# Kernel tuning notes

Measured on AMD Instinct MI355X. Metric: run time of the kernel, lower is better.

The kernel has to match this reference:

```python
import jax, jax.numpy as jnp
import numpy as np

HEADS = 2
C1 = 33    # per-head out channels, conv1
C2 = 550   # per-head out channels, conv2


def _lin_params(key, fan_in, fan_out):
    kw, kb = jax.random.split(key)
    scale = 1.0 / np.sqrt(fan_in)
    W = jax.random.uniform(kw, (fan_in, fan_out), jnp.float32, -scale, scale)
    b = jax.random.uniform(kb, (fan_out,), jnp.float32, -scale, scale)
    return W, b


def transformer_conv(x, src, dst, Wq, bq, Wk, bk, Wv, bv, Ws, bs, heads, out_ch):
    """PyG TransformerConv (concat=True, root_weight=True, beta=False)."""
    N = x.shape[0]
    q = (x @ Wq + bq).reshape(N, heads, out_ch)  # query of target node i
    k = (x @ Wk + bk).reshape(N, heads, out_ch)  # key of source node j
    v = (x @ Wv + bv).reshape(N, heads, out_ch)  # value of source node j
    # attention logits per edge: [E, H]
    alpha = jnp.einsum('ehc,ehc->eh', q[dst], k[src]) / jnp.sqrt(jnp.float32(out_ch))
    # segment softmax over incoming edges of each dst node
    m = jax.lax.stop_gradient(jax.ops.segment_max(alpha, dst, num_segments=N))  # [N,H]
    e = jnp.exp(alpha - m[dst])
    denom = jax.ops.segment_sum(e, dst, num_segments=N)  # [N,H]
    a = e / denom[dst]
    # weighted scatter-aggregate of source values: [N,H,C]
    out = jax.ops.segment_sum(a[..., None] * v[src], dst, num_segments=N)
    out = out.reshape(N, heads * out_ch)
    # root/skip connection
    out = out + x @ Ws + bs
    return out


def setup_inputs() -> dict:
    key = jax.random.key(0)
    ks = jax.random.split(key, 10)
    N, E, IN = 20000, 120000, 256
    x = jax.random.normal(ks[0], (N, IN), jnp.float32)
    edge_index = jax.random.randint(ks[1], (2, E), 0, N, jnp.int64 if jax.config.jax_enable_x64 else jnp.int32)
    d = {'x': x, 'edge_index': edge_index}
    # conv1: IN -> heads*C1
    d['Wq1'], d['bq1'] = _lin_params(ks[2], IN, HEADS * C1)
    d['Wk1'], d['bk1'] = _lin_params(ks[3], IN, HEADS * C1)
    d['Wv1'], d['bv1'] = _lin_params(ks[4], IN, HEADS * C1)
    d['Ws1'], d['bs1'] = _lin_params(ks[5], IN, HEADS * C1)
    # conv2: heads*C1 -> heads*C2
    IN2 = HEADS * C1
    d['Wq2'], d['bq2'] = _lin_params(ks[6], IN2, HEADS * C2)
    d['Wk2'], d['bk2'] = _lin_params(ks[7], IN2, HEADS * C2)
    d['Wv2'], d['bv2'] = _lin_params(ks[8], IN2, HEADS * C2)
    d['Ws2'], d['bs2'] = _lin_params(ks[9], IN2, HEADS * C2)
    return d


def reference(x, edge_index, Wq1, bq1, Wk1, bk1, Wv1, bv1, Ws1, bs1,
              Wq2, bq2, Wk2, bk2, Wv2, bv2, Ws2, bs2):
    src, dst = edge_index[0], edge_index[1]
    h = transformer_conv(x, src, dst, Wq1, bq1, Wk1, bk1, Wv1, bv1, Ws1, bs1, HEADS, C1)
    h = transformer_conv(h, src, dst, Wq2, bq2, Wk2, bk2, Wv2, bv2, Ws2, bs2, HEADS, C2)
    # x.view(N, 550, heads).max(dim=2) -- faithful to the original reshape layout
    h = h.reshape(h.shape[0], C2, HEADS)
    return jnp.max(h, axis=2)
```

## Files before the change

### kernel.cpp

```cpp
#include <hip/hip_runtime.h>
#include <math.h>

#define HEADS 2
#define C1    33
#define C2    550
#define D1    66
#define D2    1100
#define IN1   256
#define PROJW 288
#define KU    224
#define KZ    96
#define ZW    144
#define AUW   232

typedef __attribute__((ext_vector_type(8))) short bfrag;
typedef __attribute__((ext_vector_type(4))) float f32x4;

__device__ inline unsigned short f2bf(float f) {
    unsigned int u = __float_as_uint(f);
    u += 0x7FFFu + ((u >> 16) & 1u);
    return (unsigned short)(u >> 16);
}

__device__ inline int xcd_slot(int bid, int slots) {
    return (bid >> 3) + (bid & 7) * slots;
}

__global__ void k_prep1(const float* __restrict__ Wq, const float* __restrict__ bq,
                        const float* __restrict__ Wk, const float* __restrict__ bk,
                        const float* __restrict__ Wv, const float* __restrict__ bv,
                        const float* __restrict__ Ws, const float* __restrict__ bs,
                        unsigned short* __restrict__ Wt1, float* __restrict__ bcat) {
    int bid = blockIdx.x;
    int lk = bid & 3, t = bid >> 2;
    int ks = t & 7, g = t >> 3;
    int col = threadIdx.x;
    int c = g * 96 + col;
    int k0 = ks * 32 + lk * 8;
    short vals[8];
    float bia = 0.f;
    if (c < 4 * D1) {
        int m = c / D1, j = c % D1;
        const float* W; const float* B;
        switch (m) {
            case 0: W = Wq; B = bq; break;
            case 1: W = Wk; B = bk; break;
            case 2: W = Wv; B = bv; break;
            default: W = Ws; B = bs; break;
        }
        #pragma unroll
        for (int e = 0; e < 8; e++) vals[e] = (short)f2bf(W[(size_t)(k0 + e) * D1 + j]);
        bia = B[j];
    } else {
        #pragma unroll
        for (int e = 0; e < 8; e++) vals[e] = 0;
    }
    *(bfrag*)&Wt1[((size_t)bid * 96 + col) * 8] = *(bfrag*)vals;
    if (ks == 0 && lk == 0) bcat[c] = bia;
}

__global__ void k_prep2(const float* __restrict__ Wv2, const float* __restrict__ bv2,
                        const float* __restrict__ Ws2, const float* __restrict__ bs2,
                        unsigned short* __restrict__ W2t) {
    int bid = blockIdx.x;
    int lk = bid & 3, t = bid >> 2;
    int ks = t % 7, g = t / 7;
    int col = threadIdx.x;
    int c = g * 96 + col;
    int k0 = ks * 32 + lk * 8;
    short vals[8];
    #pragma unroll
    for (int e = 0; e < 8; e++) {
        int k = k0 + e;
        float val = 0.f;
        if (c < D2) {
            if (c < C2) {
                if (k < 66) val = Wv2[(size_t)k * D2 + c];
                else if (k >= 132 && k < 198) val = Ws2[(size_t)(k - 132) * D2 + c];
                else if (k == 198) val = bv2[c];
                else if (k == 223) val = bs2[c];
            } else {
                if (k >= 66 && k < 132) val = Wv2[(size_t)(k - 66) * D2 + c];
                else if (k >= 132 && k < 198) val = Ws2[(size_t)(k - 132) * D2 + c];
                else if (k == 199) val = bv2[c];
                else if (k == 223) val = bs2[c];
            }
        }
        vals[e] = (short)f2bf(val);
    }
    *(bfrag*)&W2t[((size_t)bid * 96 + col) * 8] = *(bfrag*)vals;
}

__global__ void k_hist(const int* __restrict__ dst, int E, int* __restrict__ cnt) {
    int e = blockIdx.x * blockDim.x + threadIdx.x;
    if (e < E) atomicAdd(&cnt[dst[e]], 1);
}

__global__ void k_scan(const int* __restrict__ cnt, int* __restrict__ roff,
                       int* __restrict__ pos, int N) {
    __shared__ int wsum[16];
    __shared__ int carry_s;
    int tid = threadIdx.x, wid = tid >> 6, lane = tid & 63;
    if (tid == 0) { carry_s = 0; roff[0] = 0; }
    __syncthreads();
    for (int base = 0; base < N; base += 1024) {
        int i = base + tid;
        int v = (i < N) ? cnt[i] : 0;
        int x = v;
        #pragma unroll
        for (int s = 1; s < 64; s <<= 1) {
            int t = __shfl_up(x, s, 64);
            if (lane >= s) x += t;
        }
        if (lane == 63) wsum[wid] = x;
        __syncthreads();
        if (tid < 16) {
            int y = wsum[tid];
            #pragma unroll
            for (int s = 1; s < 16; s <<= 1) {
                int t = __shfl_up(y, s, 16);
                if (tid >= s) y += t;
            }
            wsum[tid] = y;
        }
        __syncthreads();
        int carry = carry_s;
        int incl = carry + (wid ? wsum[wid - 1] : 0) + x;
        if (i < N) { roff[i + 1] = incl; pos[i] = incl - v; }
        __syncthreads();
        if (tid == 0) carry_s = carry + wsum[15];
        __syncthreads();
    }
}

__global__ void k_fill(const int* __restrict__ src, const int* __restrict__ dst, int E,
                       int* __restrict__ pos, int* __restrict__ elist) {
    int e = blockIdx.x * blockDim.x + threadIdx.x;
    if (e < E) {
        int slot = atomicAdd(&pos[dst[e]], 1);
        elist[slot] = src[e];
    }
}

__global__ __launch_bounds__(256) void k_precomp(
        const float* __restrict__ Wq2, const float* __restrict__ bq2,
        const float* __restrict__ Wk2, const float* __restrict__ bk2,
        unsigned short* __restrict__ GBt, float* __restrict__ cc) {
    int wave = threadIdx.x >> 6, lane = threadIdx.x & 63;
    int j = blockIdx.x * 4 + wave;
    if (j >= 8978) return;
    const float *u, *v;
    int h = 0, a = 0, b = 0;
    if (j < 8976) {
        h = j / 4488;
        int r = j % 4488;
        a = r / 68; b = r % 68;
        if (b < 66)      { u = Wq2 + (size_t)a * D2 + h * C2; v = Wk2 + (size_t)b * D2 + h * C2; }
        else if (b == 66){ u = Wq2 + (size_t)a * D2 + h * C2; v = bk2 + h * C2; }
        else             { u = Wk2 + (size_t)a * D2 + h * C2; v = bq2 + h * C2; }
    } else {
        h = j - 8976;
        u = bq2 + h * C2; v = bk2 + h * C2;
    }
    float acc = 0.f;
    for (int c = lane; c < C2; c += 64) acc += u[c] * v[c];
    #pragma unroll
    for (int off = 32; off >= 1; off >>= 1) acc += __shfl_xor(acc, off, 64);
    if (lane == 0) {
        if (j < 8976) {
            int r, k;
            if (b < 66)      { r = h * 66 + a; k = b; }
            else if (b == 66){ r = 132 + h;    k = a; }
            else             { r = 134 + h;    k = a; }
            int g = r / 96, cm = r % 96;
            int ks2 = k >> 5, rem = k & 31, lk2 = rem >> 3, e = rem & 7;
            GBt[(((size_t)(g * 3 + ks2) * 4 + lk2) * 96 + cm) * 8 + e] = f2bf(acc);
        } else {
            cc[h] = acc;
        }
    }
}

__global__ __launch_bounds__(256) void k_mm1(
        const float* __restrict__ X, const unsigned short* __restrict__ B,
        const float* __restrict__ bias, float* __restrict__ proj, int N,
        int nRow, int slots) {
    int s = xcd_slot(blockIdx.x, slots);
    if (s >= nRow * 3) return;
    int rowt = s / 3, g = s - rowt * 3;
    int cbase = g * 96;
    int wave = threadIdx.x >> 6, lane = threadIdx.x & 63;
    int lr = lane & 15, lk = lane >> 4;
    int rbase = rowt * 128 + wave * 32;
    int ar[2];
    #pragma unroll
    for (int mi = 0; mi < 2; mi++) {
        int r = rbase + mi * 16 + lr;
        ar[mi] = (r < N) ? r : (N - 1);
    }
    bfrag a[2][8];
    #pragma unroll
    for (int mi = 0; mi < 2; mi++)
        #pragma unroll
        for (int ks = 0; ks < 8; ks++) {
            const float* p = X + (size_t)ar[mi] * IN1 + ks * 32 + lk * 8;
            float4 v0 = *(const float4*)p;
            float4 v1 = *(const float4*)(p + 4);
            bfrag r;
            r[0] = (short)f2bf(v0.x); r[1] = (short)f2bf(v0.y);
            r[2] = (short)f2bf(v0.z); r[3] = (short)f2bf(v0.w);
            r[4] = (short)f2bf(v1.x); r[5] = (short)f2bf(v1.y);
            r[6] = (short)f2bf(v1.z); r[7] = (short)f2bf(v1.w);
            a[mi][ks] = r;
        }
    f32x4 acc[2][6];
    #pragma unroll
    for (int mi = 0; mi < 2; mi++)
        #pragma unroll
        for (int ni = 0; ni < 6; ni++) acc[mi][ni] = (f32x4){0.f, 0.f, 0.f, 0.f};
    #pragma unroll
    for (int ks = 0; ks < 8; ks++) {
        bfrag b[6];
        #pragma unroll
        for (int ni = 0; ni < 6; ni++)
            b[ni] = *(const bfrag*)(B + (size_t)(g * 8 + ks) * 3072 + lk * 768 + (ni * 16 + lr) * 8);
        #pragma unroll
        for (int mi = 0; mi < 2; mi++)
            #pragma unroll
            for (int ni = 0; ni < 6; ni++)
                acc[mi][ni] = __builtin_amdgcn_mfma_f32_16x16x32_bf16(a[mi][ks], b[ni], acc[mi][ni], 0, 0, 0);
    }
    #pragma unroll
    for (int mi = 0; mi < 2; mi++) {
        #pragma unroll
        for (int ni = 0; ni < 6; ni++) {
            int col = cbase + ni * 16 + lr;
            float bia = bias[col];
            #pragma unroll
            for (int r = 0; r < 4; r++) {
                int row = rbase + mi * 16 + lk * 4 + r;
                if (row < N) proj[(size_t)row * PROJW + col] = acc[mi][ni][r] + bia;
            }
        }
    }
}

__global__ __launch_bounds__(128) void k_conv1(
        const float* __restrict__ proj, const int* __restrict__ roff,
        const int* __restrict__ elist, float* __restrict__ h1,
        unsigned short* __restrict__ h1b, int N) {
    int n = blockIdx.x;
    int h = threadIdx.x >> 6;
    int lane = threadIdx.x & 63;
    int half = lane >> 5, l32 = lane & 31;
    size_t pb = (size_t)n * PROJW;
    int hc = h * C1;
    float q_a = proj[pb + hc + l32];
    float q_b = (l32 == 0) ? proj[pb + hc + 32] : 0.f;
    int E0 = roff[n], E1 = roff[n + 1];
    float m = -INFINITY, lsum = 0.f, aca = 0.f, acb = 0.f;
    const float isc = 0.17407765595569785f;
    int i = E0 + half;
    for (; i + 2 < E1; i += 4) {
        int s0 = elist[i], s1 = elist[i + 2];
        size_t b0 = (size_t)s0 * PROJW, b1 = (size_t)s1 * PROJW;
        float k0a = proj[b0 + 66 + hc + l32];
        float k0b = (l32 == 0) ? proj[b0 + 66 + hc + 32] : 0.f;
        float k1a = proj[b1 + 66 + hc + l32];
        float k1b = (l32 == 0) ? proj[b1 + 66 + hc + 32] : 0.f;
        float v0a = proj[b0 + 132 + hc + l32];
        float v0b = (l32 == 0) ? proj[b0 + 132 + hc + 32] : 0.f;
        float v1a = proj[b1 + 132 + hc + l32];
        float v1b = (l32 == 0) ? proj[b1 + 132 + hc + 32] : 0.f;
        float p0 = q_a * k0a + q_b * k0b;
        float p1 = q_a * k1a + q_b * k1b;
        #pragma unroll
        for (int off = 16; off >= 1; off >>= 1) {
            p0 += __shfl_xor(p0, off, 32);
            p1 += __shfl_xor(p1, off, 32);
        }
        float a0 = p0 * isc, a1 = p1 * isc;
        float mp = fmaxf(a0, a1);
        float e0 = __expf(a0 - mp), e1 = __expf(a1 - mp);
        float lp = e0 + e1;
        float apa = e0 * v0a + e1 * v1a;
        float apb = e0 * v0b + e1 * v1b;
        float mnew = fmaxf(m, mp);
        float sc = __expf(m - mnew), sp = __expf(mp - mnew);
        lsum = lsum * sc + lp * sp;
        aca = aca * sc + apa * sp;
        acb = acb * sc + apb * sp;
        m = mnew;
    }
    for (; i < E1; i += 2) {
        int s = elist[i];
        size_t sb = (size_t)s * PROJW;
        float ka = proj[sb + 66 + hc + l32];
        float kb = (l32 == 0) ? proj[sb + 66 + hc + 32] : 0.f;
        float va = proj[sb + 132 + hc + l32];
        float vb = (l32 == 0) ? proj[sb + 132 + hc + 32] : 0.f;
        float p = q_a * ka + q_b * kb;
        #pragma unroll
        for (int off = 16; off >= 1; off >>= 1) p += __shfl_xor(p, off, 32);
        float alpha = p * isc;
        float mnew = fmaxf(m, alpha);
        float sc = __expf(m - mnew);
        float pe = __expf(alpha - mnew);
        lsum = lsum * sc + pe;
        aca = aca * sc + pe * va;
        acb = acb * sc + pe * vb;
        m = mnew;
    }
    float mO  = __shfl_xor(m, 32, 64);
    float lO  = __shfl_xor(lsum, 32, 64);
    float aaO = __shfl_xor(aca, 32, 64);
    float abO = __shfl_xor(acb, 32, 64);
    float mnew = fmaxf(m, mO);
    float sS = (m  > -INFINITY) ? __expf(m  - mnew) : 0.f;
    float sO = (mO > -INFINITY) ? __expf(mO - mnew) : 0.f;
    lsum = lsum * sS + lO * sO;
    aca  = aca * sS + aaO * sO;
    acb  = acb * sS + abO * sO;
    float inv = (lsum > 0.f) ? 1.f / lsum : 0.f;
    if (half == 0) {
        float s1a = proj[pb + 198 + hc + l32];
        float val = aca * inv + s1a;
        h1[(size_t)n * D1 + hc + l32] = val;
        h1b[(size_t)n * KZ + hc + l32] = f2bf(val);
        if (l32 == 0) {
            float s1b = proj[pb + 198 + hc + 32];
            float valb = acb * inv + s1b;
            h1[(size_t)n * D1 + hc + 32] = valb;
            h1b[(size_t)n * KZ + hc + 32] = f2bf(valb);
        }
    } else if (h == 1 && l32 < 30) {
        h1b[(size_t)n * KZ + D1 + l32] = 0;
    }
}

__global__ __launch_bounds__(256) void k_mmz(
        const unsigned short* __restrict__ A, const unsigned short* __restrict__ B,
        float* __restrict__ Z, int N, int nRow, int slots) {
    int s = xcd_slot(blockIdx.x, slots);
    if (s >= nRow * 2) return;
    int rowt = s >> 1, g = s & 1;
    int wave = threadIdx.x >> 6, lane = threadIdx.x & 63;
    int lr = lane & 15, lk = lane >> 4;
    int rbase = rowt * 64 + (wave >> 1) * 32;
    int ch = (wave & 1) * 48;
    int cbase = g * 96 + ch;
    f32x4 acc[2][3];
    #pragma unroll
    for (int i = 0; i < 2; i++)
        #pragma unroll
        for (int j = 0; j < 3; j++) acc[i][j] = (f32x4){0.f, 0.f, 0.f, 0.f};
    int ar[2];
    #pragma unroll
    for (int mi = 0; mi < 2; mi++) {
        int r = rbase + mi * 16 + lr;
        ar[mi] = (r < N) ? r : (N - 1);
    }
    #pragma unroll
    for (int ks = 0; ks < 3; ks++) {
        bfrag a[2], b[3];
        #pragma unroll
        for (int mi = 0; mi < 2; mi++)
            a[mi] = *(const bfrag*)(A + (size_t)ar[mi] * KZ + ks * 32 + lk * 8);
        #pragma unroll
        for (int ni = 0; ni < 3; ni++)
            b[ni] = *(const bfrag*)(B + (size_t)(g * 3 + ks) * 3072 + lk * 768 + (ch + ni * 16 + lr) * 8);
        #pragma unroll
        for (int mi = 0; mi < 2; mi++)
            #pragma unroll
            for (int ni = 0; ni < 3; ni++)
                acc[mi][ni] = __builtin_amdgcn_mfma_f32_16x16x32_bf16(a[mi], b[ni], acc[mi][ni], 0, 0, 0);
    }
    #pragma unroll
    for (int mi = 0; mi < 2; mi++) {
        #pragma unroll
        for (int ni = 0; ni < 3; ni++) {
            int col = cbase + ni * 16 + lr;
            if (col >= 136) continue;
            #pragma unroll
            for (int r = 0; r < 4; r++) {
                int row = rbase + mi * 16 + lk * 4 + r;
                if (row < N) Z[(size_t)row * ZW + col] = acc[mi][ni][r];
            }
        }
    }
}

__global__ __launch_bounds__(128) void k_conv2(
        const float* __restrict__ h1, const float* __restrict__ Z,
        const float* __restrict__ cc, const int* __restrict__ roff,
        const int* __restrict__ elist, unsigned short* __restrict__ U, int N) {
    int n = blockIdx.x;
    int h = threadIdx.x >> 6;
    int lane = threadIdx.x & 63;
    int half = lane >> 5, l32 = lane & 31;
    int hD = h * D1;
    size_t nb = (size_t)n * D1;
    float hd_a = h1[nb + l32];
    float hd_b = h1[nb + 32 + l32];
    float hd_c = (l32 < 2) ? h1[nb + 64 + l32] : 0.f;
    float adv = Z[(size_t)n * ZW + 132 + h] + cc[h];
    int E0 = roff[n], E1 = roff[n + 1];
    float m = -INFINITY, lsum = 0.f, aa = 0.f, ab = 0.f, ac = 0.f;
    const float isc = 0.04264014327112209f;
    int i = E0 + half;
    for (; i + 2 < E1; i += 4) {
        int s0 = elist[i], s1 = elist[i + 2];
        const float* z0 = Z + (size_t)s0 * ZW;
        const float* z1 = Z + (size_t)s1 * ZW;
        float z0c = (l32 < 2) ? z0[hD + 64 + l32] : 0.f;
        float z1c = (l32 < 2) ? z1[hD + 64 + l32] : 0.f;
        float p0 = hd_a * z0[hD + l32] + hd_b * z0[hD + 32 + l32] + hd_c * z0c;
        float p1 = hd_a * z1[hD + l32] + hd_b * z1[hD + 32 + l32] + hd_c * z1c;
        float as0 = z0[134 + h], as1 = z1[134 + h];
        #pragma unroll
        for (int off = 16; off >= 1; off >>= 1) {
            p0 += __shfl_xor(p0, off, 32);
            p1 += __shfl_xor(p1, off, 32);
        }
        float al0 = (p0 + adv + as0) * isc;
        float al1 = (p1 + adv + as1) * isc;
        size_t v0b = (size_t)s0 * D1, v1b = (size_t)s1 * D1;
        float v0a = h1[v0b + l32], v0bb = h1[v0b + 32 + l32];
        float v0c = (l32 < 2) ? h1[v0b + 64 + l32] : 0.f;
        float v1a = h1[v1b + l32], v1bb = h1[v1b + 32 + l32];
        float v1c = (l32 < 2) ? h1[v1b + 64 + l32] : 0.f;
        float mp = fmaxf(al0, al1);
        float e0 = __expf(al0 - mp), e1 = __expf(al1 - mp);
        float lp = e0 + e1;
        float mnew = fmaxf(m, mp);
        float sc = __expf(m - mnew), sp = __expf(mp - mnew);
        lsum = lsum * sc + lp * sp;
        aa = aa * sc + (e0 * v0a + e1 * v1a) * sp;
        ab = ab * sc + (e0 * v0bb + e1 * v1bb) * sp;
        ac = ac * sc + (e0 * v0c + e1 * v1c) * sp;
        m = mnew;
    }
    for (; i < E1; i += 2) {
        int s = elist[i];
        const float* zr = Z + (size_t)s * ZW;
        float zc = (l32 < 2) ? zr[hD + 64 + l32] : 0.f;
        float p = hd_a * zr[hD + l32] + hd_b * zr[hD + 32 + l32] + hd_c * zc;
        float as_ = zr[134 + h];
        #pragma unroll
        for (int off = 16; off >= 1; off >>= 1) p += __shfl_xor(p, off, 32);
        float alpha = (p + adv + as_) * isc;
        size_t vb = (size_t)s * D1;
        float va = h1[vb + l32], vbb = h1[vb + 32 + l32];
        float vc = (l32 < 2) ? h1[vb + 64 + l32] : 0.f;
        float mnew = fmaxf(m, alpha);
        float sc = __expf(m - mnew);
        float pe = __expf(alpha - mnew);
        lsum = lsum * sc + pe;
        aa = aa * sc + pe * va;
        ab = ab * sc + pe * vbb;
        ac = ac * sc + pe * vc;
        m = mnew;
    }
    float mO  = __shfl_xor(m, 32, 64);
    float lO  = __shfl_xor(lsum, 32, 64);
    float aaO = __shfl_xor(aa, 32, 64);
    float abO = __shfl_xor(ab, 32, 64);
    float acO = __shfl_xor(ac, 32, 64);
    float mnew = fmaxf(m, mO);
    float sS = (m  > -INFINITY) ? __expf(m  - mnew) : 0.f;
    float sO = (mO > -INFINITY) ? __expf(mO - mnew) : 0.f;
    lsum = lsum * sS + lO * sO;
    aa = aa * sS + aaO * sO;
    ab = ab * sS + abO * sO;
    ac = ac * sS + acO * sO;
    float inv = (lsum > 0.f) ? 1.f / lsum : 0.f;
    size_t ub = (size_t)n * KU;
    if (half == 0) {
        U[ub + hD + l32] = f2bf(aa * inv);
        if (l32 < 2) U[ub + hD + 64 + l32] = f2bf(ac * inv);
    } else {
        U[ub + hD + 32 + l32] = f2bf(ab * inv);
    }
    if (lane == 0) U[ub + 198 + h] = (lsum > 0.f) ? (unsigned short)0x3F80 : (unsigned short)0;
    if (h == 0) {
        if (half == 0) {
            U[ub + 132 + l32] = f2bf(hd_a);
            if (l32 < 2) U[ub + 132 + 64 + l32] = f2bf(hd_c);
            if (l32 == 2) U[ub + 223] = (unsigned short)0x3F80;
        } else {
            U[ub + 132 + 32 + l32] = f2bf(hd_b);
        }
    } else if (half == 1 && l32 < 23) {
        U[ub + 200 + l32] = 0;
    }
}

__global__ __launch_bounds__(256) void k_mm2(
        const unsigned short* __restrict__ A, const unsigned short* __restrict__ B,
        float* __restrict__ out, int N, int nRow, int slots) {
    __shared__ __align__(16) char smem[128 * AUW * 2];
    unsigned short (*au)[AUW] = (unsigned short (*)[AUW])smem;
    float (*ot)[32][49] = (float (*)[32][49])smem;
    int s = xcd_slot(blockIdx.x, slots);
    if (s >= nRow * 12) return;
    int rowt = s / 12, g = s - rowt * 12;
    int tid = threadIdx.x;
    int rbb = rowt * 128;
    #pragma unroll
    for (int it = 0; it < 14; it++) {
        int i = it * 256 + tid;
        int row = i / 28, ch = i - row * 28;
        int gr = rbb + row; if (gr >= N) gr = N - 1;
        *(bfrag*)&au[row][ch * 8] = *(const bfrag*)(A + (size_t)gr * KU + ch * 8);
    }
    int wave = tid >> 6, lane = tid & 63;
    int lr = lane & 15, lk = lane >> 4;
    int rbase = rbb + wave * 32;
    __syncthreads();
    bfrag a[2][7];
    #pragma unroll
    for (int mi = 0; mi < 2; mi++)
        #pragma unroll
        for (int ks = 0; ks < 7; ks++)
            a[mi][ks] = *(const bfrag*)&au[wave * 32 + mi * 16 + lr][ks * 32 + lk * 8];
    f32x4 acc[2][6];
    #pragma unroll
    for (int mi = 0; mi < 2; mi++)
        #pragma unroll
        for (int ni = 0; ni < 6; ni++) acc[mi][ni] = (f32x4){0.f, 0.f, 0.f, 0.f};
    #pragma unroll
    for (int ks = 0; ks < 7; ks++) {
        bfrag b[6];
        #pragma unroll
        for (int ni = 0; ni < 6; ni++)
            b[ni] = *(const bfrag*)(B + (size_t)(g * 7 + ks) * 3072 + lk * 768 + (ni * 16 + lr) * 8);
        #pragma unroll
        for (int mi = 0; mi < 2; mi++)
            #pragma unroll
            for (int ni = 0; ni < 6; ni++)
                acc[mi][ni] = __builtin_amdgcn_mfma_f32_16x16x32_bf16(a[mi][ks], b[ni], acc[mi][ni], 0, 0, 0);
    }
    __syncthreads();
    #pragma unroll
    for (int mi = 0; mi < 2; mi++) {
        #pragma unroll
        for (int ni = 0; ni < 6; ni++) {
            #pragma unroll
            for (int r = 0; r < 4; r++) {
                float val = acc[mi][ni][r];
                float oth = __shfl_xor(val, 1, 64);
                if (!(lane & 1))
                    ot[wave][mi * 16 + lk * 4 + r][ni * 8 + (lr >> 1)] = fmaxf(val, oth);
            }
        }
    }
    __syncthreads();
    int colb = g * 48;
    #pragma unroll
    for (int i = 0; i < 24; i++) {
        int t = i * 64 + lane;
        int r32 = t / 48, pos = t - r32 * 48;
        int row = rbase + r32;
        int col = colb + pos;
        if (row < N && col < C2)
            out[(size_t)row * C2 + col] = ot[wave][r32][pos];
    }
}

extern "C" void kernel_launch(void* const* d_in, const int* in_sizes, int n_in,
                              void* d_out, int out_size, void* d_ws, size_t ws_size,
                              hipStream_t stream) {
    const float* x  = (const float*)d_in[0];
    const int*   ei = (const int*)d_in[1];
    int N = in_sizes[0] / IN1;
    int E = in_sizes[1] / 2;
    const int* src = ei;
    const int* dst = ei + E;

    const float *Wq1 = (const float*)d_in[2],  *bq1 = (const float*)d_in[3];
    const float *Wk1 = (const float*)d_in[4],  *bk1 = (const float*)d_in[5];
    const float *Wv1 = (const float*)d_in[6],  *bv1 = (const float*)d_in[7];
    const float *Ws1 = (const float*)d_in[8],  *bs1 = (const float*)d_in[9];
    const float *Wq2 = (const float*)d_in[10], *bq2 = (const float*)d_in[11];
    const float *Wk2 = (const float*)d_in[12], *bk2 = (const float*)d_in[13];
    const float *Wv2 = (const float*)d_in[14], *bv2 = (const float*)d_in[15];
    const float *Ws2 = (const float*)d_in[16], *bs2 = (const float*)d_in[17];

    char* w = (char*)d_ws;
    size_t off = 0;
    auto take = [&](size_t bytes) { size_t o = off; off = (off + bytes + 255) & ~(size_t)255; return o; };

    size_t proj_off = take((size_t)N * PROJW * 4);
    float* proj = (float*)(w + proj_off);
    float* Z = proj;
    unsigned short* U = (unsigned short*)(w + proj_off + (size_t)N * ZW * 4);
    float* h1   = (float*)(w + take((size_t)N * D1 * 4));
    unsigned short* h1b = (unsigned short*)(w + take((size_t)N * KZ * 2));
    float* cc   = (float*)(w + take(2 * 4));
    unsigned short* GBt = (unsigned short*)(w + take((size_t)24 * 96 * 8 * 2));
    unsigned short* Wt1 = (unsigned short*)(w + take((size_t)96 * 96 * 8 * 2));
    float* bcat = (float*)(w + take(PROJW * 4));
    unsigned short* W2t = (unsigned short*)(w + take((size_t)336 * 96 * 8 * 2));
    int* cnt   = (int*)(w + take((size_t)N * 4));
    int* roff  = (int*)(w + take((size_t)(N + 1) * 4));
    int* pos   = (int*)(w + take((size_t)N * 4));
    int* elist = (int*)(w + take((size_t)E * 4));

    hipMemsetAsync(cnt, 0, (size_t)N * sizeof(int), stream);
    k_hist<<<(E + 255) / 256, 256, 0, stream>>>(dst, E, cnt);
    k_scan<<<1, 1024, 0, stream>>>(cnt, roff, pos, N);
    k_fill<<<(E + 255) / 256, 256, 0, stream>>>(src, dst, E, pos, elist);

    k_prep1<<<96, 96, 0, stream>>>(Wq1, bq1, Wk1, bk1, Wv1, bv1, Ws1, bs1, Wt1, bcat);
    k_prep2<<<336, 96, 0, stream>>>(Wv2, bv2, Ws2, bs2, W2t);
    k_precomp<<<(8978 + 3) / 4, 256, 0, stream>>>(Wq2, bq2, Wk2, bk2, GBt, cc);

    int nRow1 = (N + 127) / 128;
    int tot1  = nRow1 * 3;
    int slots1 = (tot1 + 7) / 8;
    int nRowZ = (N + 63) / 64;
    int totZ  = nRowZ * 2;
    int slotsZ = (totZ + 7) / 8;
    int nRow2 = (N + 127) / 128;
    int tot2  = nRow2 * 12;
    int slots2 = (tot2 + 7) / 8;

    k_mm1<<<slots1 * 8, 256, 0, stream>>>(x, Wt1, bcat, proj, N, nRow1, slots1);
    k_conv1<<<N, 128, 0, stream>>>(proj, roff, elist, h1, h1b, N);

    k_mmz<<<slotsZ * 8, 256, 0, stream>>>(h1b, GBt, Z, N, nRowZ, slotsZ);

    k_conv2<<<N, 128, 0, stream>>>(h1, Z, cc, roff, elist, U, N);

    k_mm2<<<slots2 * 8, 256, 0, stream>>>(U, W2t, (float*)d_out, N, nRow2, slots2);
}
```

Baseline: 175.7 us.

## Merge setup kernels into combined launches and load mm2 A-fragments directly

Combines the histogram, both weight-prep kernels and the Wq2·Wk2 precompute into one launch, selecting the role by block-index range. It also merges the CSR fill with the first projection GEMM, cutting the number of serialized kernel launches and the gaps between them. Separately, k_mm2 stops staging the A tile through shared memory and reads the bf16 fragments straight from global memory, which removes a barrier and LDS traffic. The cost is that the A loads are no longer coalesced the same way, and the merged kernels now run 96-thread jobs in 256-thread blocks, leaving some threads idle.

```diff
diff --git a/kernel.cpp b/kernel.cpp
--- a/kernel.cpp
+++ b/kernel.cpp
@@ -11,7 +11,6 @@
 #define KU    224
 #define KZ    96
 #define ZW    144
-#define AUW   232
 
 typedef __attribute__((ext_vector_type(8))) short bfrag;
 typedef __attribute__((ext_vector_type(4))) float f32x4;
@@ -26,74 +25,123 @@
     return (bid >> 3) + (bid & 7) * slots;
 }
 
-__global__ void k_prep1(const float* __restrict__ Wq, const float* __restrict__ bq,
-                        const float* __restrict__ Wk, const float* __restrict__ bk,
-                        const float* __restrict__ Wv, const float* __restrict__ bv,
-                        const float* __restrict__ Ws, const float* __restrict__ bs,
-                        unsigned short* __restrict__ Wt1, float* __restrict__ bcat) {
+__global__ __launch_bounds__(256) void k_mega(
+        const int* __restrict__ dst, int E, int* __restrict__ cnt, int histBlocks,
+        const float* __restrict__ Wq1, const float* __restrict__ bq1,
+        const float* __restrict__ Wk1, const float* __restrict__ bk1,
+        const float* __restrict__ Wv1, const float* __restrict__ bv1,
+        const float* __restrict__ Ws1, const float* __restrict__ bs1,
+        unsigned short* __restrict__ Wt1, float* __restrict__ bcat,
+        const float* __restrict__ Wv2, const float* __restrict__ bv2,
+        const float* __restrict__ Ws2, const float* __restrict__ bs2,
+        unsigned short* __restrict__ W2t,
+        const float* __restrict__ Wq2, const float* __restrict__ bq2,
+        const float* __restrict__ Wk2, const float* __restrict__ bk2,
+        unsigned short* __restrict__ GBt, float* __restrict__ cc) {
     int bid = blockIdx.x;
-    int lk = bid & 3, t = bid >> 2;
-    int ks = t & 7, g = t >> 3;
-    int col = threadIdx.x;
-    int c = g * 96 + col;
-    int k0 = ks * 32 + lk * 8;
-    short vals[8];
-    float bia = 0.f;
-    if (c < 4 * D1) {
-        int m = c / D1, j = c % D1;
-        const float* W; const float* B;
-        switch (m) {
-            case 0: W = Wq; B = bq; break;
-            case 1: W = Wk; B = bk; break;
-            case 2: W = Wv; B = bv; break;
-            default: W = Ws; B = bs; break;
-        }
-        #pragma unroll
-        for (int e = 0; e < 8; e++) vals[e] = (short)f2bf(W[(size_t)(k0 + e) * D1 + j]);
-        bia = B[j];
-    } else {
-        #pragma unroll
-        for (int e = 0; e < 8; e++) vals[e] = 0;
-    }
-    *(bfrag*)&Wt1[((size_t)bid * 96 + col) * 8] = *(bfrag*)vals;
-    if (ks == 0 && lk == 0) bcat[c] = bia;
-}
-
-__global__ void k_prep2(const float* __restrict__ Wv2, const float* __restrict__ bv2,
-                        const float* __restrict__ Ws2, const float* __restrict__ bs2,
-                        unsigned short* __restrict__ W2t) {
-    int bid = blockIdx.x;
-    int lk = bid & 3, t = bid >> 2;
-    int ks = t % 7, g = t / 7;
-    int col = threadIdx.x;
-    int c = g * 96 + col;
-    int k0 = ks * 32 + lk * 8;
-    short vals[8];
-    #pragma unroll
-    for (int e = 0; e < 8; e++) {
-        int k = k0 + e;
-        float val = 0.f;
-        if (c < D2) {
-            if (c < C2) {
-                if (k < 66) val = Wv2[(size_t)k * D2 + c];
-                else if (k >= 132 && k < 198) val = Ws2[(size_t)(k - 132) * D2 + c];
-                else if (k == 198) val = bv2[c];
-                else if (k == 223) val = bs2[c];
+    int tid = threadIdx.x;
+    if (bid < histBlocks) {
+        int e = bid * 256 + tid;
+        if (e < E) atomicAdd(&cnt[dst[e]], 1);
+        return;
+    }
+    bid -= histBlocks;
+    if (bid < 96) {
+        if (tid >= 96) return;
+        int lk = bid & 3, t = bid >> 2;
+        int ks = t & 7, g = t >> 3;
+        int col = tid;
+        int c = g * 96 + col;
+        int k0 = ks * 32 + lk * 8;
+        short vals[8];
+        float bia = 0.f;
+        if (c < 4 * D1) {
+            int m = c / D1, j = c % D1;
+            const float* W; const float* B;
+            switch (m) {
+                case 0: W = Wq1; B = bq1; break;
+                case 1: W = Wk1; B = bk1; break;
+                case 2: W = Wv1; B = bv1; break;
+                default: W = Ws1; B = bs1; break;
+            }
+            #pragma unroll
+            for (int e = 0; e < 8; e++) vals[e] = (short)f2bf(W[(size_t)(k0 + e) * D1 + j]);
+            bia = B[j];
+        } else {
+            #pragma unroll
+            for (int e = 0; e < 8; e++) vals[e] = 0;
+        }
+        *(bfrag*)&Wt1[((size_t)bid * 96 + col) * 8] = *(bfrag*)vals;
+        if (ks == 0 && lk == 0) bcat[c] = bia;
+        return;
+    }
+    bid -= 96;
+    if (bid < 336) {
+        if (tid >= 96) return;
+        int lk = bid & 3, t = bid >> 2;
+        int ks = t % 7, g = t / 7;
+        int col = tid;
+        int c = g * 96 + col;
+        int k0 = ks * 32 + lk * 8;
+        short vals[8];
+        #pragma unroll
+        for (int e = 0; e < 8; e++) {
+            int k = k0 + e;
+            float val = 0.f;
+            if (c < D2) {
+                if (c < C2) {
+                    if (k < 66) val = Wv2[(size_t)k * D2 + c];
+                    else if (k >= 132 && k < 198) val = Ws2[(size_t)(k - 132) * D2 + c];
+                    else if (k == 198) val = bv2[c];
+                    else if (k == 223) val = bs2[c];
+                } else {
+                    if (k >= 66 && k < 132) val = Wv2[(size_t)(k - 66) * D2 + c];
+                    else if (k >= 132 && k < 198) val = Ws2[(size_t)(k - 132) * D2 + c];
+                    else if (k == 199) val = bv2[c];
+                    else if (k == 223) val = bs2[c];
+                }
+            }
+            vals[e] = (short)f2bf(val);
+        }
+        *(bfrag*)&W2t[((size_t)bid * 96 + col) * 8] = *(bfrag*)vals;
+        return;
+    }
+    bid -= 336;
+    {
+        int wave = tid >> 6, lane = tid & 63;
+        int j = bid * 4 + wave;
+        if (j >= 8978) return;
+        const float *u, *v;
+        int h = 0, a = 0, b = 0;
+        if (j < 8976) {
+            h = j / 4488;
+            int r = j % 4488;
+            a = r / 68; b = r % 68;
+            if (b < 66)      { u = Wq2 + (size_t)a * D2 + h * C2; v = Wk2 + (size_t)b * D2 + h * C2; }
+            else if (b == 66){ u = Wq2 + (size_t)a * D2 + h * C2; v = bk2 + h * C2; }
+            else             { u = Wk2 + (size_t)a * D2 + h * C2; v = bq2 + h * C2; }
+        } else {
+            h = j - 8976;
+            u = bq2 + h * C2; v = bk2 + h * C2;
+        }
+        float acc = 0.f;
+        for (int c = lane; c < C2; c += 64) acc += u[c] * v[c];
+        #pragma unroll
+        for (int off = 32; off >= 1; off >>= 1) acc += __shfl_xor(acc, off, 64);
+        if (lane == 0) {
+            if (j < 8976) {
+                int r, k;
+                if (b < 66)      { r = h * 66 + a; k = b; }
+                else if (b == 66){ r = 132 + h;    k = a; }
+                else             { r = 134 + h;    k = a; }
+                int g = r / 96, cm = r % 96;
+                int ks2 = k >> 5, rem = k & 31, lk2 = rem >> 3, e = rem & 7;
+                GBt[(((size_t)(g * 3 + ks2) * 4 + lk2) * 96 + cm) * 8 + e] = f2bf(acc);
             } else {
-                if (k >= 66 && k < 132) val = Wv2[(size_t)(k - 66) * D2 + c];
-                else if (k >= 132 && k < 198) val = Ws2[(size_t)(k - 132) * D2 + c];
-                else if (k == 199) val = bv2[c];
-                else if (k == 223) val = bs2[c];
+                cc[h] = acc;
             }
         }
-        vals[e] = (short)f2bf(val);
-    }
-    *(bfrag*)&W2t[((size_t)bid * 96 + col) * 8] = *(bfrag*)vals;
-}
-
-__global__ void k_hist(const int* __restrict__ dst, int E, int* __restrict__ cnt) {
-    int e = blockIdx.x * blockDim.x + threadIdx.x;
-    if (e < E) atomicAdd(&cnt[dst[e]], 1);
+    }
 }
 
 __global__ void k_scan(const int* __restrict__ cnt, int* __restrict__ roff,
@@ -133,63 +181,28 @@
     }
 }
 
-__global__ void k_fill(const int* __restrict__ src, const int* __restrict__ dst, int E,
-                       int* __restrict__ pos, int* __restrict__ elist) {
-    int e = blockIdx.x * blockDim.x + threadIdx.x;
-    if (e < E) {
-        int slot = atomicAdd(&pos[dst[e]], 1);
-        elist[slot] = src[e];
-    }
-}
-
-__global__ __launch_bounds__(256) void k_precomp(
-        const float* __restrict__ Wq2, const float* __restrict__ bq2,
-        const float* __restrict__ Wk2, const float* __restrict__ bk2,
-        unsigned short* __restrict__ GBt, float* __restrict__ cc) {
-    int wave = threadIdx.x >> 6, lane = threadIdx.x & 63;
-    int j = blockIdx.x * 4 + wave;
-    if (j >= 8978) return;
-    const float *u, *v;
-    int h = 0, a = 0, b = 0;
-    if (j < 8976) {
-        h = j / 4488;
-        int r = j % 4488;
-        a = r / 68; b = r % 68;
-        if (b < 66)      { u = Wq2 + (size_t)a * D2 + h * C2; v = Wk2 + (size_t)b * D2 + h * C2; }
-        else if (b == 66){ u = Wq2 + (size_t)a * D2 + h * C2; v = bk2 + h * C2; }
-        else             { u = Wk2 + (size_t)a * D2 + h * C2; v = bq2 + h * C2; }
-    } else {
-        h = j - 8976;
-        u = bq2 + h * C2; v = bk2 + h * C2;
-    }
-    float acc = 0.f;
-    for (int c = lane; c < C2; c += 64) acc += u[c] * v[c];
-    #pragma unroll
-    for (int off = 32; off >= 1; off >>= 1) acc += __shfl_xor(acc, off, 64);
-    if (lane == 0) {
-        if (j < 8976) {
-            int r, k;
-            if (b < 66)      { r = h * 66 + a; k = b; }
-            else if (b == 66){ r = 132 + h;    k = a; }
-            else             { r = 134 + h;    k = a; }
-            int g = r / 96, cm = r % 96;
-            int ks2 = k >> 5, rem = k & 31, lk2 = rem >> 3, e = rem & 7;
-            GBt[(((size_t)(g * 3 + ks2) * 4 + lk2) * 96 + cm) * 8 + e] = f2bf(acc);
-        } else {
-            cc[h] = acc;
-        }
-    }
-}
-
-__global__ __launch_bounds__(256) void k_mm1(
+__global__ __launch_bounds__(256) void k_fillmm1(
+        const int* __restrict__ src, const int* __restrict__ dst, int E,
+        int* __restrict__ pos, int* __restrict__ elist, int fillBlocks,
         const float* __restrict__ X, const unsigned short* __restrict__ B,
         const float* __restrict__ bias, float* __restrict__ proj, int N,
         int nRow, int slots) {
-    int s = xcd_slot(blockIdx.x, slots);
+    int bid = blockIdx.x;
+    int tid = threadIdx.x;
+    if (bid < fillBlocks) {
+        int e = bid * 256 + tid;
+        if (e < E) {
+            int slot = atomicAdd(&pos[dst[e]], 1);
+            elist[slot] = src[e];
+        }
+        return;
+    }
+    bid -= fillBlocks;
+    int s = xcd_slot(bid, slots);
     if (s >= nRow * 3) return;
     int rowt = s / 3, g = s - rowt * 3;
     int cbase = g * 96;
-    int wave = threadIdx.x >> 6, lane = threadIdx.x & 63;
+    int wave = tid >> 6, lane = tid & 63;
     int lr = lane & 15, lk = lane >> 4;
     int rbase = rowt * 128 + wave * 32;
     int ar[2];
@@ -498,31 +511,25 @@
 __global__ __launch_bounds__(256) void k_mm2(
         const unsigned short* __restrict__ A, const unsigned short* __restrict__ B,
         float* __restrict__ out, int N, int nRow, int slots) {
-    __shared__ __align__(16) char smem[128 * AUW * 2];
-    unsigned short (*au)[AUW] = (unsigned short (*)[AUW])smem;
-    float (*ot)[32][49] = (float (*)[32][49])smem;
+    __shared__ float ot[4][32][49];
     int s = xcd_slot(blockIdx.x, slots);
     if (s >= nRow * 12) return;
     int rowt = s / 12, g = s - rowt * 12;
-    int tid = threadIdx.x;
-    int rbb = rowt * 128;
-    #pragma unroll
-    for (int it = 0; it < 14; it++) {
-        int i = it * 256 + tid;
-        int row = i / 28, ch = i - row * 28;
-        int gr = rbb + row; if (gr >= N) gr = N - 1;
-        *(bfrag*)&au[row][ch * 8] = *(const bfrag*)(A + (size_t)gr * KU + ch * 8);
-    }
-    int wave = tid >> 6, lane = tid & 63;
+    int wave = threadIdx.x >> 6, lane = threadIdx.x & 63;
     int lr = lane & 15, lk = lane >> 4;
-    int rbase = rbb + wave * 32;
-    __syncthreads();
+    int rbase = rowt * 128 + wave * 32;
+    int ar[2];
+    #pragma unroll
+    for (int mi = 0; mi < 2; mi++) {
+        int r = rbase + mi * 16 + lr;
+        ar[mi] = (r < N) ? r : (N - 1);
+    }
     bfrag a[2][7];
     #pragma unroll
     for (int mi = 0; mi < 2; mi++)
         #pragma unroll
         for (int ks = 0; ks < 7; ks++)
-            a[mi][ks] = *(const bfrag*)&au[wave * 32 + mi * 16 + lr][ks * 32 + lk * 8];
+            a[mi][ks] = *(const bfrag*)(A + (size_t)ar[mi] * KU + ks * 32 + lk * 8);
     f32x4 acc[2][6];
     #pragma unroll
     for (int mi = 0; mi < 2; mi++)
@@ -540,7 +547,6 @@
             for (int ni = 0; ni < 6; ni++)
                 acc[mi][ni] = __builtin_amdgcn_mfma_f32_16x16x32_bf16(a[mi][ks], b[ni], acc[mi][ni], 0, 0, 0);
     }
-    __syncthreads();
     #pragma unroll
     for (int mi = 0; mi < 2; mi++) {
         #pragma unroll
@@ -606,15 +612,7 @@
     int* pos   = (int*)(w + take((size_t)N * 4));
     int* elist = (int*)(w + take((size_t)E * 4));
 
-    hipMemsetAsync(cnt, 0, (size_t)N * sizeof(int), stream);
-    k_hist<<<(E + 255) / 256, 256, 0, stream>>>(dst, E, cnt);
-    k_scan<<<1, 1024, 0, stream>>>(cnt, roff, pos, N);
-    k_fill<<<(E + 255) / 256, 256, 0, stream>>>(src, dst, E, pos, elist);
-
-    k_prep1<<<96, 96, 0, stream>>>(Wq1, bq1, Wk1, bk1, Wv1, bv1, Ws1, bs1, Wt1, bcat);
-    k_prep2<<<336, 96, 0, stream>>>(Wv2, bv2, Ws2, bs2, W2t);
-    k_precomp<<<(8978 + 3) / 4, 256, 0, stream>>>(Wq2, bq2, Wk2, bk2, GBt, cc);
-
+    int histBlocks = (E + 255) / 256;
     int nRow1 = (N + 127) / 128;
     int tot1  = nRow1 * 3;
     int slots1 = (tot1 + 7) / 8;
@@ -625,7 +623,20 @@
     int tot2  = nRow2 * 12;
     int slots2 = (tot2 + 7) / 8;
 
-    k_mm1<<<slots1 * 8, 256, 0, stream>>>(x, Wt1, bcat, proj, N, nRow1, slots1);
+    hipMemsetAsync(cnt, 0, (size_t)N * sizeof(int), stream);
+
+    k_mega<<<histBlocks + 96 + 336 + 2245, 256, 0, stream>>>(
+        dst, E, cnt, histBlocks,
+        Wq1, bq1, Wk1, bk1, Wv1, bv1, Ws1, bs1, Wt1, bcat,
+        Wv2, bv2, Ws2, bs2, W2t,
+        Wq2, bq2, Wk2, bk2, GBt, cc);
+
+    k_scan<<<1, 1024, 0, stream>>>(cnt, roff, pos, N);
+
+    k_fillmm1<<<histBlocks + slots1 * 8, 256, 0, stream>>>(
+        src, dst, E, pos, elist, histBlocks,
+        x, Wt1, bcat, proj, N, nRow1, slots1);
+
     k_conv1<<<N, 128, 0, stream>>>(proj, roff, elist, h1, h1b, N);
 
     k_mmz<<<slotsZ * 8, 256, 0, stream>>>(h1b, GBt, Z, N, nRowZ, slotsZ);
```

Measured after the change: 162.9 us. 1.08x faster.
